# Kernel optimization log

Measured on AMD Instinct MI355X. Metric: run time of the kernel, lower is better.

## Reference

```python
import math
import jax, jax.numpy as jnp
import numpy as np

CAPACITY_FACTOR = 1.0

def setup_inputs() -> dict:
    key = jax.random.key(0)
    k1, k2 = jax.random.split(key)
    token_input = jax.random.normal(k1, (4096, 1024), dtype=jnp.float32)
    wg2_weight = jax.random.normal(k2, (64, 1024), dtype=jnp.float32) * 0.02
    return {"token_input": token_input, "wg2_weight": wg2_weight}

def reference(token_input, wg2_weight):
    S, _ = token_input.shape
    E = wg2_weight.shape[0]
    num_2nd = E // 4
    capacity = int(2 * math.ceil(S / num_2nd) * CAPACITY_FACTOR)  # static
    eps = jnp.finfo(jnp.float32).eps

    logits = token_input @ wg2_weight.T               # [S, E]
    gates = jax.nn.softmax(logits, axis=-1)           # [S, E]

    # top-1 expert
    idx1 = jnp.argmax(gates, axis=1)                  # [S]
    mask1 = jax.nn.one_hot(idx1, E, dtype=jnp.int32)  # [S, E]

    # second expert via gumbel sampling on the gate values (masked-out top1)
    gumbel = jax.random.gumbel(jax.random.key(42), gates.shape, dtype=jnp.float32)
    noisy = gates + gumbel
    masked = jnp.where(mask1.astype(bool), -jnp.inf, noisy)
    idx2 = jnp.argmax(masked, axis=1)
    mask2 = jax.nn.one_hot(idx2, E, dtype=jnp.int32)

    # cumsum-based slot locations (fused_cumsum_sub_one)
    locations1 = jnp.cumsum(mask1, axis=0) - 1                       # [S, E]
    locations2 = jnp.cumsum(mask2, axis=0) - 1 + jnp.sum(mask1, axis=0, keepdims=True)

    # load-balance aux loss
    me = jnp.mean(gates, axis=0)
    ce = jnp.mean(mask1.astype(gates.dtype), axis=0)
    l_aux = jnp.sum(me * ce) / num_2nd * (E * E)

    # capacity dropping
    mask1 = mask1 * (locations1 < capacity).astype(jnp.int32)
    mask2 = mask2 * (locations2 < capacity).astype(jnp.int32)

    # gate probs renormalized over kept assignments
    gates1_s = jnp.sum(gates * mask1, axis=1)
    gates2_s = jnp.sum(gates * mask2, axis=1)
    denom = jnp.maximum(gates1_s + gates2_s, eps)
    gates1_s = gates1_s / denom
    gates2_s = gates2_s / denom

    loc1_s = jnp.sum(locations1 * mask1, axis=1)      # [S]
    loc2_s = jnp.sum(locations2 * mask2, axis=1)

    gates1 = gates1_s[:, None] * mask1.astype(gates.dtype)  # [S, E]
    gates2 = gates2_s[:, None] * mask2.astype(gates.dtype)

    loc1_sc = jax.nn.one_hot(loc1_s, capacity, dtype=gates.dtype)  # [S, C]
    loc2_sc = jax.nn.one_hot(loc2_s, capacity, dtype=gates.dtype)

    combine_weights = (jnp.einsum('se,sc->sec', gates1, loc1_sc)
                       + jnp.einsum('se,sc->sec', gates2, loc2_sc))  # [S, E, C]
    dispatch_mask = combine_weights > 0
    return l_aux, combine_weights, dispatch_mask
```

## Files before the change

### kernel.cpp

```cpp
#include <hip/hip_runtime.h>
#include <math.h>
#include <stdint.h>

#define S_TOK 4096
#define N_EXP 64
#define MDIM  1024
#define TB    8
#define CAP   512
#define NBLK_GATE (S_TOK / TB)

struct TokRec { int idx1; int idx2; float g1; float g2; };

__device__ __forceinline__ void tf4(uint32_t& x0, uint32_t& x1,
                                    int r0, int r1, int r2, int r3) {
  x0 += x1; x1 = (x1 << r0) | (x1 >> (32 - r0)); x1 ^= x0;
  x0 += x1; x1 = (x1 << r1) | (x1 >> (32 - r1)); x1 ^= x0;
  x0 += x1; x1 = (x1 << r2) | (x1 >> (32 - r2)); x1 ^= x0;
  x0 += x1; x1 = (x1 << r3) | (x1 >> (32 - r3)); x1 ^= x0;
}

__device__ __forceinline__ float jax_gumbel(uint32_t f) {
  const uint32_t k0 = 0u, k1 = 42u;
  const uint32_t k2 = 0x1BD11BDAu ^ 42u;
  uint32_t x0 = 0u + k0;
  uint32_t x1 = f + k1;
  tf4(x0, x1, 13, 15, 26,  6); x0 += k1; x1 += k2 + 1u;
  tf4(x0, x1, 17, 29, 16, 24); x0 += k2; x1 += k0 + 2u;
  tf4(x0, x1, 13, 15, 26,  6); x0 += k0; x1 += k1 + 3u;
  tf4(x0, x1, 17, 29, 16, 24); x0 += k1; x1 += k2 + 4u;
  tf4(x0, x1, 13, 15, 26,  6); x0 += k2; x1 += k0 + 5u;
  uint32_t bits = x0 ^ x1;
  float u = __uint_as_float((bits >> 9) | 0x3F800000u) - 1.0f;
  u = fmaxf(u, 1.17549435e-38f);
  return -logf(-logf(u));
}

__global__ __launch_bounds__(256) void k_gate(const float* __restrict__ tok,
                                              const float* __restrict__ W,
                                              TokRec* __restrict__ recs,
                                              float* __restrict__ mePart) {
  __shared__ float t_lds[TB * MDIM];
  __shared__ float logits_l[TB * N_EXP];
  __shared__ float meAcc[4][N_EXP];

  const int tid  = threadIdx.x;
  const int wave = tid >> 6;
  const int lane = tid & 63;
  const int tok0 = blockIdx.x * TB;

  {
    const float4* src = (const float4*)(tok + (size_t)tok0 * MDIM);
    float4* dst = (float4*)t_lds;
    #pragma unroll
    for (int i = 0; i < (TB * MDIM / 4) / 256; ++i)
      dst[tid + i * 256] = src[tid + i * 256];
  }
  __syncthreads();

  for (int p = 0; p < N_EXP / 4; ++p) {
    const int e = p * 4 + wave;
    const float* wr = W + (size_t)e * MDIM;
    float acc[TB];
    #pragma unroll
    for (int t = 0; t < TB; ++t) acc[t] = 0.f;
    for (int k = lane; k < MDIM; k += 64) {
      float wv = wr[k];
      #pragma unroll
      for (int t = 0; t < TB; ++t) acc[t] = fmaf(t_lds[t * MDIM + k], wv, acc[t]);
    }
    #pragma unroll
    for (int t = 0; t < TB; ++t) {
      float v = acc[t];
      #pragma unroll
      for (int o = 32; o >= 1; o >>= 1) v += __shfl_xor(v, o, 64);
      if (lane == 0) logits_l[t * N_EXP + e] = v;
    }
  }
  __syncthreads();

  const int e = lane;
  float meLocal = 0.f;
  #pragma unroll
  for (int rep = 0; rep < 2; ++rep) {
    const int t = wave + rep * 4;
    const int s = tok0 + t;
    float x = logits_l[t * N_EXP + e];
    float m = x;
    #pragma unroll
    for (int o = 32; o >= 1; o >>= 1) m = fmaxf(m, __shfl_xor(m, o, 64));
    float ex = expf(x - m);
    float sum = ex;
    #pragma unroll
    for (int o = 32; o >= 1; o >>= 1) sum += __shfl_xor(sum, o, 64);
    float gate = ex / sum;
    meLocal += gate;

    float bv = gate; int bi = e;
    #pragma unroll
    for (int o = 32; o >= 1; o >>= 1) {
      float ov = __shfl_xor(bv, o, 64);
      int   oi = __shfl_xor(bi, o, 64);
      if (ov > bv || (ov == bv && oi < bi)) { bv = ov; bi = oi; }
    }
    const int idx1 = bi;

    float noisy = (e == idx1) ? -INFINITY
                              : (gate + jax_gumbel((uint32_t)(s * N_EXP + e)));
    float bv2 = noisy; int bi2 = e;
    #pragma unroll
    for (int o = 32; o >= 1; o >>= 1) {
      float ov = __shfl_xor(bv2, o, 64);
      int   oi = __shfl_xor(bi2, o, 64);
      if (ov > bv2 || (ov == bv2 && oi < bi2)) { bv2 = ov; bi2 = oi; }
    }
    const int idx2 = bi2;

    float g1 = __shfl(gate, idx1, 64);
    float g2 = __shfl(gate, idx2, 64);
    if (lane == 0) {
      TokRec r; r.idx1 = idx1; r.idx2 = idx2; r.g1 = g1; r.g2 = g2;
      recs[s] = r;
    }
  }
  meAcc[wave][e] = meLocal;
  __syncthreads();
  if (wave == 0)
    mePart[(size_t)blockIdx.x * N_EXP + e] =
        meAcc[0][e] + meAcc[1][e] + meAcc[2][e] + meAcc[3][e];
}

__global__ __launch_bounds__(1024) void k_finish(const TokRec* __restrict__ recs,
                                                 const float* __restrict__ mePart,
                                                 float* __restrict__ out) {
  __shared__ unsigned short pk_l[S_TOK];
  __shared__ unsigned short rank1_l[S_TOK];
  __shared__ unsigned short rank2_l[S_TOK];
  __shared__ int   cnt1[16][N_EXP];
  __shared__ int   cnt2[16][N_EXP];
  __shared__ int   off1[16][N_EXP];
  __shared__ int   off2[16][N_EXP];
  __shared__ int   total1_l[N_EXP];
  __shared__ float meAcc[16][N_EXP];
  __shared__ float laux_l[N_EXP];

  const int tid  = threadIdx.x;
  const int wave = tid >> 6;
  const int lane = tid & 63;

  for (int s = tid; s < S_TOK; s += 1024) {
    TokRec r = recs[s];
    pk_l[s] = (unsigned short)(r.idx1 | (r.idx2 << 8));
  }
  __syncthreads();

  {
    int c1 = 0, c2 = 0;
    const int s0 = wave * (S_TOK / 16);
    for (int j = 0; j < S_TOK / 16; ++j) {
      const int s = s0 + j;
      const int v  = pk_l[s];
      const int v1 = v & 0xFF;
      const int v2 = v >> 8;
      if (v1 == lane) { rank1_l[s] = (unsigned short)c1; ++c1; }
      if (v2 == lane) { rank2_l[s] = (unsigned short)c2; ++c2; }
    }
    cnt1[wave][lane] = c1;
    cnt2[wave][lane] = c2;
  }
  __syncthreads();

  if (tid < N_EXP) {
    int off = 0;
    #pragma unroll
    for (int w = 0; w < 16; ++w) { off1[w][tid] = off; off += cnt1[w][tid]; }
    total1_l[tid] = off;
    int o2 = off;
    #pragma unroll
    for (int w = 0; w < 16; ++w) { off2[w][tid] = o2; o2 += cnt2[w][tid]; }
  }
  __syncthreads();

  float* comb = out + 1;
  float* mask = out + 1 + (size_t)S_TOK * N_EXP * CAP;
  for (int s = tid; s < S_TOK; s += 1024) {
    TokRec r = recs[s];
    const int w  = s / (S_TOK / 16);
    const int l1 = (int)rank1_l[s] + off1[w][r.idx1];
    const int l2 = (int)rank2_l[s] + off2[w][r.idx2];
    const bool k1 = l1 < CAP;
    const bool k2 = l2 < CAP;
    float g1 = k1 ? r.g1 : 0.f;
    float g2 = k2 ? r.g2 : 0.f;
    float denom = fmaxf(g1 + g2, 1.1920929e-07f);
    float g1n = g1 / denom;
    float g2n = g2 / denom;
    const size_t base = (size_t)s * N_EXP * CAP;
    if (k1) { size_t o = base + (size_t)r.idx1 * CAP + l1; comb[o] = g1n; mask[o] = 1.0f; }
    if (k2) { size_t o = base + (size_t)r.idx2 * CAP + l2; comb[o] = g2n; mask[o] = 1.0f; }
  }

  {
    float a = 0.f;
    for (int b = wave; b < NBLK_GATE; b += 16) a += mePart[(size_t)b * N_EXP + lane];
    meAcc[wave][lane] = a;
  }
  __syncthreads();
  if (tid < N_EXP) {
    float sg = 0.f;
    #pragma unroll
    for (int w = 0; w < 16; ++w) sg += meAcc[w][tid];
    laux_l[tid] = sg * (float)total1_l[tid];
  }
  __syncthreads();
  if (tid == 0) {
    float t = 0.f;
    for (int e2 = 0; e2 < N_EXP; ++e2) t += laux_l[e2];
    out[0] = t * (1.0f / 65536.0f);
  }
}

extern "C" void kernel_launch(void* const* d_in, const int* in_sizes, int n_in,
                              void* d_out, int out_size, void* d_ws, size_t ws_size,
                              hipStream_t stream) {
  const float* tok = (const float*)d_in[0];
  const float* W   = (const float*)d_in[1];
  float* out = (float*)d_out;

  TokRec* recs   = (TokRec*)d_ws;
  float*  mePart = (float*)((char*)d_ws + S_TOK * sizeof(TokRec));

  const size_t out_bytes = ((size_t)S_TOK * N_EXP * CAP * 2 + 1) * sizeof(float);
  hipMemsetAsync(out, 0, out_bytes, stream);

  k_gate  <<<NBLK_GATE, 256, 0, stream>>>(tok, W, recs, mePart);
  k_finish<<<1, 1024, 0, stream>>>(recs, mePart, out);
}
```

Measured before the change: 1.186 ms.

## Replace memset plus scatter with single dense nontemporal output write kernel

The full-output hipMemsetAsync and the scattered writes from a single-block finish kernel are replaced. The finish kernel now emits compact per-token write records, and a new grid-wide kernel writes every output element once, as zero or the kept value, using vectorized nontemporal stores. This avoids writing the large combine/mask tensors twice and moves the sparse stores out of one block. It adds a third kernel launch and extra workspace, and it has to handle the odd offset of 1 float at the start of the output.

```diff
diff --git a/kernel.cpp b/kernel.cpp
--- a/kernel.cpp
+++ b/kernel.cpp
@@ -9,7 +9,13 @@
 #define CAP   512
 #define NBLK_GATE (S_TOK / TB)
 
-struct TokRec { int idx1; int idx2; float g1; float g2; };
+#define SEC      ((size_t)S_TOK * N_EXP * CAP)
+#define TOKSLAB  (N_EXP * CAP)
+
+struct TokRec   { int idx1; int idx2; float g1; float g2; };
+struct WriteRec { int f1; int f2; float g1; float g2; };
+
+typedef float f4v __attribute__((ext_vector_type(4)));
 
 __device__ __forceinline__ void tf4(uint32_t& x0, uint32_t& x1,
                                     int r0, int r1, int r2, int r3) {
@@ -129,9 +135,10 @@
         meAcc[0][e] + meAcc[1][e] + meAcc[2][e] + meAcc[3][e];
 }
 
-__global__ __launch_bounds__(1024) void k_finish(const TokRec* __restrict__ recs,
-                                                 const float* __restrict__ mePart,
-                                                 float* __restrict__ out) {
+__global__ __launch_bounds__(1024) void k_rank(const TokRec* __restrict__ recs,
+                                               const float* __restrict__ mePart,
+                                               WriteRec* __restrict__ wrecs,
+                                               float* __restrict__ laux_ws) {
   __shared__ unsigned short pk_l[S_TOK];
   __shared__ unsigned short rank1_l[S_TOK];
   __shared__ unsigned short rank2_l[S_TOK];
@@ -180,8 +187,6 @@
   }
   __syncthreads();
 
-  float* comb = out + 1;
-  float* mask = out + 1 + (size_t)S_TOK * N_EXP * CAP;
   for (int s = tid; s < S_TOK; s += 1024) {
     TokRec r = recs[s];
     const int w  = s / (S_TOK / 16);
@@ -192,11 +197,12 @@
     float g1 = k1 ? r.g1 : 0.f;
     float g2 = k2 ? r.g2 : 0.f;
     float denom = fmaxf(g1 + g2, 1.1920929e-07f);
-    float g1n = g1 / denom;
-    float g2n = g2 / denom;
-    const size_t base = (size_t)s * N_EXP * CAP;
-    if (k1) { size_t o = base + (size_t)r.idx1 * CAP + l1; comb[o] = g1n; mask[o] = 1.0f; }
-    if (k2) { size_t o = base + (size_t)r.idx2 * CAP + l2; comb[o] = g2n; mask[o] = 1.0f; }
+    WriteRec o;
+    o.f1 = k1 ? (r.idx1 * CAP + l1) : -1;
+    o.f2 = k2 ? (r.idx2 * CAP + l2) : -1;
+    o.g1 = g1 / denom;
+    o.g2 = g2 / denom;
+    wrecs[s] = o;
   }
 
   {
@@ -215,7 +221,53 @@
   if (tid == 0) {
     float t = 0.f;
     for (int e2 = 0; e2 < N_EXP; ++e2) t += laux_l[e2];
-    out[0] = t * (1.0f / 65536.0f);
+    laux_ws[0] = t * (1.0f / 65536.0f);
+  }
+}
+
+__global__ __launch_bounds__(256) void k_write(const WriteRec* __restrict__ wrecs,
+                                               const float* __restrict__ laux_ws,
+                                               float* __restrict__ out) {
+  const int s   = blockIdx.x;
+  const int tid = threadIdx.x;
+  const WriteRec w = wrecs[s];
+  float* cb = out + 1 + (size_t)s * TOKSLAB;
+  float* mb = cb + SEC;
+
+  if (s == 0 && tid == 0) out[0] = laux_ws[0];
+
+  if (tid < 3) {
+    float cv = (tid == w.f1) ? w.g1 : ((tid == w.f2) ? w.g2 : 0.f);
+    float mv = (tid == w.f1 || tid == w.f2) ? 1.f : 0.f;
+    __builtin_nontemporal_store(cv, cb + tid);
+    __builtin_nontemporal_store(mv, mb + tid);
+  }
+
+  const f4v z = {0.f, 0.f, 0.f, 0.f};
+  #pragma unroll 4
+  for (int i = 0; i < 32; ++i) {
+    const int k = i * 256 + tid;
+    if (k < 8191) {
+      const int f0 = 3 + 4 * k;
+      f4v cv = z, mv = z;
+      const unsigned d1 = (unsigned)(w.f1 - f0);
+      const unsigned d2 = (unsigned)(w.f2 - f0);
+      if (d1 < 4u || d2 < 4u) {
+        #pragma unroll
+        for (int j = 0; j < 4; ++j) {
+          const int f = f0 + j;
+          if (f == w.f1) { cv[j] = w.g1; mv[j] = 1.f; }
+          if (f == w.f2) { cv[j] = w.g2; mv[j] = 1.f; }
+        }
+      }
+      __builtin_nontemporal_store(cv, (f4v*)(cb + f0));
+      __builtin_nontemporal_store(mv, (f4v*)(mb + f0));
+    } else {
+      float cv = (32767 == w.f1) ? w.g1 : ((32767 == w.f2) ? w.g2 : 0.f);
+      float mv = (32767 == w.f1 || 32767 == w.f2) ? 1.f : 0.f;
+      __builtin_nontemporal_store(cv, cb + 32767);
+      __builtin_nontemporal_store(mv, mb + 32767);
+    }
   }
 }
 
@@ -226,12 +278,13 @@
   const float* W   = (const float*)d_in[1];
   float* out = (float*)d_out;
 
-  TokRec* recs   = (TokRec*)d_ws;
-  float*  mePart = (float*)((char*)d_ws + S_TOK * sizeof(TokRec));
-
-  const size_t out_bytes = ((size_t)S_TOK * N_EXP * CAP * 2 + 1) * sizeof(float);
-  hipMemsetAsync(out, 0, out_bytes, stream);
-
-  k_gate  <<<NBLK_GATE, 256, 0, stream>>>(tok, W, recs, mePart);
-  k_finish<<<1, 1024, 0, stream>>>(recs, mePart, out);
-}
+  char* ws = (char*)d_ws;
+  TokRec*   recs    = (TokRec*)ws;                       ws += S_TOK * sizeof(TokRec);
+  float*    mePart  = (float*)ws;                        ws += NBLK_GATE * N_EXP * sizeof(float);
+  WriteRec* wrecs   = (WriteRec*)ws;                     ws += S_TOK * sizeof(WriteRec);
+  float*    laux_ws = (float*)ws;
+
+  k_gate <<<NBLK_GATE, 256, 0, stream>>>(tok, W, recs, mePart);
+  k_rank <<<1, 1024, 0, stream>>>(recs, mePart, wrecs, laux_ws);
+  k_write<<<S_TOK, 256, 0, stream>>>(wrecs, laux_ws, out);
+}
```

New measurement: 1.282 ms. 8.0% more time.
